# Kernel tuning notes

Hardware: AMD Instinct MI355X
Metric: run time of the kernel (lower is better)

## Reference

```python
import jax, jax.numpy as jnp
import numpy as np

LATENT, ACTION, HIDDEN, TEMB = 256, 32, 1024, 128
BATCH, NTRAJ, HORIZON = 1024, 16, 5
EPI_W, PRAG_W, CONS_W, GAMMA = 1.0, 1.0, 0.1, 0.99
LOG2PI = float(np.log(2.0 * np.pi))


def _dense_init(key, fan_in, fan_out):
    return jax.random.normal(key, (fan_in, fan_out), dtype=jnp.float32) / np.sqrt(fan_in)


def time_embed(t):
    # sinusoidal embedding, TEMB dims, like ValueNetwork(time_embed_dim=128)
    half = TEMB // 2
    freqs = jnp.exp(-np.log(10000.0) * jnp.arange(half, dtype=jnp.float32) / half)
    ang = t[:, None] * freqs[None, :]  # [B, half]
    return jnp.concatenate([jnp.sin(ang), jnp.cos(ang)], axis=-1)  # [B, TEMB]


def setup_inputs() -> dict:
    key = jax.random.key(0)
    ks = jax.random.split(key, 12)
    return {
        "latent": jax.random.normal(ks[0], (BATCH, LATENT), dtype=jnp.float32),
        "noise": jax.random.normal(ks[1], (NTRAJ, HORIZON, BATCH, ACTION), dtype=jnp.float32),
        # DiffusionConditionedPolicy (state-dependent std): trunk + mean/log_std heads
        "pW1": _dense_init(ks[2], LATENT, HIDDEN), "pb1": jnp.zeros((HIDDEN,), jnp.float32),
        "pW2": _dense_init(ks[3], HIDDEN, HIDDEN), "pb2": jnp.zeros((HIDDEN,), jnp.float32),
        "pWm": _dense_init(ks[4], HIDDEN, ACTION), "pbm": jnp.zeros((ACTION,), jnp.float32),
        "pWs": _dense_init(ks[5], HIDDEN, ACTION), "pbs": jnp.zeros((ACTION,), jnp.float32),
        # LatentDynamicsModel: 3-layer MLP on [latent, action] -> delta
        "dW1": _dense_init(ks[6], LATENT + ACTION, HIDDEN), "db1": jnp.zeros((HIDDEN,), jnp.float32),
        "dW2": _dense_init(ks[7], HIDDEN, HIDDEN), "db2": jnp.zeros((HIDDEN,), jnp.float32),
        "dW3": _dense_init(ks[8], HIDDEN, LATENT), "db3": jnp.zeros((LATENT,), jnp.float32),
        # ValueNetwork: 3-layer MLP on [latent, time_embed] -> scalar
        "vW1": _dense_init(ks[9], LATENT + TEMB, HIDDEN), "vb1": jnp.zeros((HIDDEN,), jnp.float32),
        "vW2": _dense_init(ks[10], HIDDEN, HIDDEN), "vb2": jnp.zeros((HIDDEN,), jnp.float32),
        "vW3": _dense_init(ks[11], HIDDEN, 1), "vb3": jnp.zeros((1,), jnp.float32),
    }


def _efe_forward(latent, noise, pW1, pb1, pW2, pb2, pWm, pbm, pWs, pbs,
                 dW1, db1, dW2, db2, dW3, db3, vW1, vb1, vW2, vb2, vW3, vb3):
    def policy(z, eps):
        h = jax.nn.silu(z @ pW1 + pb1)
        h = jax.nn.silu(h @ pW2 + pb2)
        mean = h @ pWm + pbm
        log_std = jnp.clip(h @ pWs + pbs, -5.0, 2.0)
        action = mean + jnp.exp(log_std) * eps  # reparameterized sample
        # Normal entropy per-dim, summed over action dim
        ent = jnp.sum(0.5 * (1.0 + LOG2PI) + log_std, axis=-1)
        return action, ent

    def dynamics(z, a):
        h = jnp.concatenate([z, a], axis=-1)
        h = jax.nn.silu(h @ dW1 + db1)
        h = jax.nn.silu(h @ dW2 + db2)
        return h @ dW3 + db3  # delta latent

    def value(z, tvec):
        h = jnp.concatenate([z, time_embed(tvec)], axis=-1)
        h = jax.nn.silu(h @ vW1 + vb1)
        h = jax.nn.silu(h @ vW2 + vb2)
        return (h @ vW3 + vb3)[..., 0]  # squeeze(-1)

    def step(z, inp):
        eps_t, t = inp
        action, ent = policy(z, eps_t)
        z_next = z + dynamics(z, action)  # predict_next_latent
        # _compute_latent_kl on normalized latents
        zn = z / (jnp.linalg.norm(z, axis=-1, keepdims=True) + 1e-8)
        pn = z_next / (jnp.linalg.norm(z_next, axis=-1, keepdims=True) + 1e-8)
        kl = 0.5 * jnp.sum((zn - pn) ** 2, axis=-1)
        epistemic = jnp.log1p(kl)
        tvec = jnp.full((z.shape[0],), 0.0, dtype=z.dtype) + t
        pragmatic = value(z_next, tvec)
        consistency = -ent
        step_efe = EPI_W * epistemic + PRAG_W * pragmatic + CONS_W * consistency
        return z_next, step_efe

    ts = jnp.arange(HORIZON, dtype=jnp.float32)

    def rollout(eps_traj):  # eps_traj: [H, B, A]
        _, efes = jax.lax.scan(step, latent, (eps_traj, ts))  # efes: [H, B]
        disc = GAMMA ** ts  # discount_factor ** t
        return jnp.sum(disc[:, None] * efes, axis=0)  # traj_efe: [B]

    traj_efe = jax.vmap(rollout)(noise)  # [NTRAJ, B]
    total_efe = jnp.mean(traj_efe, axis=0)  # sum of traj_efe / num_trajectories
    return total_efe


def reference(latent, noise, pW1, pb1, pW2, pb2, pWm, pbm, pWs, pbs,
              dW1, db1, dW2, db2, dW3, db3, vW1, vb1, vW2, vb2, vW3, vb3):
    return _efe_forward(latent, noise, pW1, pb1, pW2, pb2, pWm, pbm, pWs, pbs,
                        dW1, db1, dW2, db2, dW3, db3, vW1, vb1, vW2, vb2, vW3, vb3)
```

## Files before the change

kernel.cpp:

```cpp
#include <hip/hip_runtime.h>
#include <cstdint>
#include <cstddef>
#include <cmath>


typedef __bf16 bf16;
typedef __attribute__((ext_vector_type(8))) __bf16 bf16x8;
typedef __attribute__((ext_vector_type(4))) __bf16 bf16x4;
typedef __attribute__((ext_vector_type(4))) float f32x4;

static constexpr int BATCH = 1024, NTRAJ = 16, HORIZON = 5;
static constexpr int MR = NTRAJ * BATCH;
static constexpr float ENT_C = 1.4189385332046727f;
static constexpr float SUMDISC = 4.90099501f;

__device__ __forceinline__ void gld_lds16(const bf16* g, const bf16* l) {
  typedef __attribute__((address_space(1))) const uint32_t gq_t;
  typedef __attribute__((address_space(3))) uint32_t lq_t;
  gq_t* gp = (gq_t*)(uintptr_t)g;
  lq_t* lp = (lq_t*)(uint32_t)(uintptr_t)l;
  __builtin_amdgcn_global_load_lds(gp, lp, 16, 0, 0);
}

__device__ __forceinline__ float silu(float x) {
  return x * __builtin_amdgcn_rcpf(1.f + __expf(-x));
}

#define MFMA16(a, b, c) __builtin_amdgcn_mfma_f32_16x16x32_bf16((a), (b), (c), 0, 0, 0)

__global__ __launch_bounds__(256) void gemm128(
    const bf16* __restrict__ A, int lda, int K, const bf16* __restrict__ Bt,
    const float* __restrict__ bias, int act_cols,
    bf16* __restrict__ C1, bf16* __restrict__ C2, int ldc) {
  __shared__ alignas(16) bf16 As0[128 * 32], As1[128 * 32];
  __shared__ alignas(16) bf16 Bs0[128 * 32], Bs1[128 * 32];
  const int tid = threadIdx.x, wave = tid >> 6, lane = tid & 63;
  const int quad = lane >> 4, l16 = lane & 15;
  const int rowBlk = blockIdx.x * 128, colBlk = blockIdx.y * 128;
  const int wr = wave >> 1, wc = wave & 1;
  const int srow = lane >> 2;
  const int skel = (((lane & 3) ^ ((lane >> 3) & 3)) * 8);
  const int qsw = quad ^ ((l16 >> 1) & 3);

  const bf16* gA0 = A + (size_t)(rowBlk + wave * 32 + srow) * lda + skel;
  const bf16* gA1 = gA0 + (size_t)16 * lda;
  const bf16* gB0 = Bt + (size_t)(colBlk + wave * 32 + srow) * K + skel;
  const bf16* gB1 = gB0 + (size_t)16 * K;
  bf16* const lA0 = As0 + wave * 32 * 32;
  bf16* const lA0b = As0 + (wave * 32 + 16) * 32;
  bf16* const lA1 = As1 + wave * 32 * 32;
  bf16* const lA1b = As1 + (wave * 32 + 16) * 32;
  bf16* const lB0 = Bs0 + wave * 32 * 32;
  bf16* const lB0b = Bs0 + (wave * 32 + 16) * 32;
  bf16* const lB1 = Bs1 + wave * 32 * 32;
  bf16* const lB1b = Bs1 + (wave * 32 + 16) * 32;

  f32x4 acc[4][4] = {};
  for (int k0 = 0; k0 < K; k0 += 64) {
    gld_lds16(gA0 + k0, lA0);
    gld_lds16(gA1 + k0, lA0b);
    gld_lds16(gA0 + k0 + 32, lA1);
    gld_lds16(gA1 + k0 + 32, lA1b);
    gld_lds16(gB0 + k0, lB0);
    gld_lds16(gB1 + k0, lB0b);
    gld_lds16(gB0 + k0 + 32, lB1);
    gld_lds16(gB1 + k0 + 32, lB1b);
    __syncthreads();
#pragma unroll
    for (int ks = 0; ks < 2; ++ks) {
      const bf16* aRd = (ks ? As1 : As0) + (wr * 64 + l16) * 32 + qsw * 8;
      const bf16* bRd = (ks ? Bs1 : Bs0) + (wc * 64 + l16) * 32 + qsw * 8;
      bf16x8 af[4], bfr[4];
#pragma unroll
      for (int i = 0; i < 4; ++i) {
        af[i] = *(const bf16x8*)(aRd + i * 16 * 32);
        bfr[i] = *(const bf16x8*)(bRd + i * 16 * 32);
      }
#pragma unroll
      for (int mi = 0; mi < 4; ++mi)
#pragma unroll
        for (int ni = 0; ni < 4; ++ni)
          acc[mi][ni] = MFMA16(bfr[ni], af[mi], acc[mi][ni]);
    }
    __syncthreads();
  }

  const bool doAct = (colBlk < act_cols);
  bf16* const Cp = doAct ? C1 : C2;
  const int cShift = doAct ? 0 : act_cols;
#pragma unroll
  for (int mi = 0; mi < 4; ++mi) {
    const int row = rowBlk + wr * 64 + mi * 16 + l16;
#pragma unroll
    for (int ni = 0; ni < 4; ++ni) {
      const int col0 = colBlk + wc * 64 + ni * 16 + quad * 4;
      const f32x4 bb = *(const f32x4*)(bias + col0);
      bf16x4 o;
#pragma unroll
      for (int r = 0; r < 4; ++r) {
        float x = acc[mi][ni][r] + bb[r];
        if (doAct) x = silu(x);
        o[r] = (bf16)x;
      }
      *(bf16x4*)(Cp + (size_t)row * ldc + (col0 - cShift)) = o;
    }
  }
}

__global__ __launch_bounds__(256) void gemm_pd1v(
    const bf16* __restrict__ A, const bf16* __restrict__ Bt,
    const float* __restrict__ pdb1, const float* __restrict__ vbiasT,
    bf16* __restrict__ Ha, bf16* __restrict__ Hp, bf16* __restrict__ Hv) {
  __shared__ alignas(16) bf16 As0[128 * 32], As1[128 * 32];
  __shared__ alignas(16) bf16 Bs0[128 * 32], Bs1[128 * 32];
  const int tid = threadIdx.x, wave = tid >> 6, lane = tid & 63;
  const int quad = lane >> 4, l16 = lane & 15;
  const int rowBlk = blockIdx.x * 128, colBlk = blockIdx.y * 128;
  const int wr = wave >> 1, wc = wave & 1;
  const int srow = lane >> 2;
  const int skel = (((lane & 3) ^ ((lane >> 3) & 3)) * 8);
  const int qsw = quad ^ ((l16 >> 1) & 3);

  const bf16* gA0 = A + (size_t)(rowBlk + wave * 32 + srow) * 256 + skel;
  const bf16* gA1 = gA0 + (size_t)16 * 256;
  const bf16* gB0 = Bt + (size_t)(colBlk + wave * 32 + srow) * 256 + skel;
  const bf16* gB1 = gB0 + (size_t)16 * 256;
  bf16* const lA0 = As0 + wave * 32 * 32;
  bf16* const lA0b = As0 + (wave * 32 + 16) * 32;
  bf16* const lA1 = As1 + wave * 32 * 32;
  bf16* const lA1b = As1 + (wave * 32 + 16) * 32;
  bf16* const lB0 = Bs0 + wave * 32 * 32;
  bf16* const lB0b = Bs0 + (wave * 32 + 16) * 32;
  bf16* const lB1 = Bs1 + wave * 32 * 32;
  bf16* const lB1b = Bs1 + (wave * 32 + 16) * 32;

  f32x4 acc[4][4] = {};
  for (int k0 = 0; k0 < 256; k0 += 64) {
    gld_lds16(gA0 + k0, lA0);
    gld_lds16(gA1 + k0, lA0b);
    gld_lds16(gA0 + k0 + 32, lA1);
    gld_lds16(gA1 + k0 + 32, lA1b);
    gld_lds16(gB0 + k0, lB0);
    gld_lds16(gB1 + k0, lB0b);
    gld_lds16(gB0 + k0 + 32, lB1);
    gld_lds16(gB1 + k0 + 32, lB1b);
    __syncthreads();
#pragma unroll
    for (int ks = 0; ks < 2; ++ks) {
      const bf16* aRd = (ks ? As1 : As0) + (wr * 64 + l16) * 32 + qsw * 8;
      const bf16* bRd = (ks ? Bs1 : Bs0) + (wc * 64 + l16) * 32 + qsw * 8;
      bf16x8 af[4], bfr[4];
#pragma unroll
      for (int i = 0; i < 4; ++i) {
        af[i] = *(const bf16x8*)(aRd + i * 16 * 32);
        bfr[i] = *(const bf16x8*)(bRd + i * 16 * 32);
      }
#pragma unroll
      for (int mi = 0; mi < 4; ++mi)
#pragma unroll
        for (int ni = 0; ni < 4; ++ni)
          acc[mi][ni] = MFMA16(bfr[ni], af[mi], acc[mi][ni]);
    }
    __syncthreads();
  }

  const int seg = colBlk >> 10;
  bf16* const Cp = (seg == 0) ? Ha : (seg == 1) ? Hp : Hv;
  const int cShift = seg << 10;
  const float* const bp = (seg == 2) ? (vbiasT - 2048) : pdb1;
#pragma unroll
  for (int mi = 0; mi < 4; ++mi) {
    const int row = rowBlk + wr * 64 + mi * 16 + l16;
#pragma unroll
    for (int ni = 0; ni < 4; ++ni) {
      const int col0 = colBlk + wc * 64 + ni * 16 + quad * 4;
      const f32x4 bb = *(const f32x4*)(bp + col0);
      bf16x4 o;
#pragma unroll
      for (int r = 0; r < 4; ++r) {
        float x = acc[mi][ni][r] + bb[r];
        if (seg != 1) x = silu(x);
        o[r] = (bf16)x;
      }
      *(bf16x4*)(Cp + (size_t)row * 1024 + (col0 - cShift)) = o;
    }
  }
}

template <int NT, int EPI>
__global__ __launch_bounds__(512, 2) void gemm256(
    const bf16* __restrict__ A, const bf16* __restrict__ Bt, int nCol,
    const float* __restrict__ bias, const float* __restrict__ aux,
    bf16* __restrict__ C1, float* __restrict__ efe, float disc) {
  static_assert(NT >= 2, "need at least 2 K-tiles");
  constexpr int K = NT * 64;
  __shared__ alignas(16) bf16 sAB[2][2][256 * 64];

  const int tid = threadIdx.x, wave = tid >> 6, lane = tid & 63;
  const int quad = lane >> 4, l16 = lane & 15;
  const int wr = wave >> 2, wc = wave & 3;

  const int nwg = gridDim.x, flat = blockIdx.x;
  const int lid = (flat & 7) * (nwg >> 3) + (flat >> 3);
  const int rowBlk = (lid / nCol) * 256, colBlk = (lid % nCol) * 256;

  const int j8 = lane >> 3;
  const int c16e = ((lane & 7) ^ j8) * 8;
  const bf16* gAs = A + (size_t)(rowBlk + wave * 16 + j8) * K + c16e;
  const bf16* gBs = Bt + (size_t)(colBlk + wave * 16 + j8) * K + c16e;

#define STAGE_A(hh, tt, bb)                                           \
  do {                                                                \
    const bf16* g_ = gAs + (hh) * 128 * K + (tt) * 64;                \
    bf16* l_ = &sAB[(bb)][0][((hh) * 128 + wave * 16) * 64];          \
    gld_lds16(g_, l_);                                                \
    gld_lds16(g_ + 8 * K, l_ + 8 * 64);                               \
  } while (0)
#define STAGE_B(hh, tt, bb)                                           \
  do {                                                                \
    const bf16* g_ = gBs + (hh) * 128 * K + (tt) * 64;                \
    bf16* l_ = &sAB[(bb)][1][((hh) * 128 + wave * 16) * 64];          \
    gld_lds16(g_, l_);                                                \
    gld_lds16(g_ + 8 * K, l_ + 8 * 64);                               \
  } while (0)

  const int k0x = (quad * 8) ^ ((l16 & 7) << 3);
  const int aOff = (wr * 128 + l16) * 64 + k0x;
  const int bOff = (wc * 64 + l16) * 64 + k0x;

  bf16x8 bAf[4][2], bBf[2][2], bB2f[2][2];
  f32x4 acc[8][4] = {};

  STAGE_A(0, 0, 0);
  STAGE_A(1, 0, 0);
  STAGE_B(0, 0, 0);
  STAGE_B(1, 0, 0);
  STAGE_B(0, 1, 1);
  STAGE_B(1, 1, 1);
  asm volatile("s_waitcnt vmcnt(4)" ::: "memory");
  __builtin_amdgcn_s_barrier();
  __builtin_amdgcn_sched_barrier(0);

#pragma unroll 2
  for (int t = 0; t < NT; ++t) {
    const int buf = t & 1;
    const bf16* lA = &sAB[buf][0][0];
    const bf16* lB = &sAB[buf][1][0];

#pragma unroll
    for (int m = 0; m < 4; ++m)
#pragma unroll
      for (int ks = 0; ks < 2; ++ks)
        bAf[m][ks] = *(const bf16x8*)(lA + ((aOff + m * 1024) ^ (ks << 5)));
#pragma unroll
    for (int n = 0; n < 2; ++n)
#pragma unroll
      for (int ks = 0; ks < 2; ++ks)
        bBf[n][ks] = *(const bf16x8*)(lB + ((bOff + n * 1024) ^ (ks << 5)));
    if (t + 1 < NT) STAGE_A(0, t + 1, buf ^ 1);
    __builtin_amdgcn_s_barrier();
    asm volatile("s_waitcnt lgkmcnt(0)" ::: "memory");
    __builtin_amdgcn_sched_barrier(0);
    __builtin_amdgcn_s_setprio(1);
#pragma unroll
    for (int ks = 0; ks < 2; ++ks)
#pragma unroll
      for (int m = 0; m < 4; ++m)
#pragma unroll
        for (int n = 0; n < 2; ++n)
          acc[m][n] = MFMA16(bBf[n][ks], bAf[m][ks], acc[m][n]);
    __builtin_amdgcn_s_setprio(0);
    __builtin_amdgcn_s_barrier();
    __builtin_amdgcn_sched_barrier(0);

#pragma unroll
    for (int n = 0; n < 2; ++n)
#pragma unroll
      for (int ks = 0; ks < 2; ++ks)
        bB2f[n][ks] =
            *(const bf16x8*)(lB + ((bOff + (n + 2) * 1024) ^ (ks << 5)));
    if (t + 1 < NT) STAGE_A(1, t + 1, buf ^ 1);
    __builtin_amdgcn_s_barrier();
    asm volatile("s_waitcnt lgkmcnt(0)" ::: "memory");
    __builtin_amdgcn_sched_barrier(0);
    __builtin_amdgcn_s_setprio(1);
#pragma unroll
    for (int ks = 0; ks < 2; ++ks)
#pragma unroll
      for (int m = 0; m < 4; ++m)
#pragma unroll
        for (int n = 0; n < 2; ++n)
          acc[m][n + 2] = MFMA16(bB2f[n][ks], bAf[m][ks], acc[m][n + 2]);
    __builtin_amdgcn_s_setprio(0);
    __builtin_amdgcn_s_barrier();
    __builtin_amdgcn_sched_barrier(0);

#pragma unroll
    for (int m = 0; m < 4; ++m)
#pragma unroll
      for (int ks = 0; ks < 2; ++ks)
        bAf[m][ks] =
            *(const bf16x8*)(lA + ((aOff + (m + 4) * 1024) ^ (ks << 5)));
    if (t + 2 < NT) STAGE_B(0, t + 2, buf);
    __builtin_amdgcn_s_barrier();
    asm volatile("s_waitcnt lgkmcnt(0)" ::: "memory");
    __builtin_amdgcn_sched_barrier(0);
    __builtin_amdgcn_s_setprio(1);
#pragma unroll
    for (int ks = 0; ks < 2; ++ks)
#pragma unroll
      for (int m = 0; m < 4; ++m)
#pragma unroll
        for (int n = 0; n < 2; ++n)
          acc[m + 4][n + 2] =
              MFMA16(bB2f[n][ks], bAf[m][ks], acc[m + 4][n + 2]);
    __builtin_amdgcn_s_setprio(0);
    __builtin_amdgcn_s_barrier();
    __builtin_amdgcn_sched_barrier(0);

    if (t + 2 < NT) STAGE_B(1, t + 2, buf);
    __builtin_amdgcn_s_barrier();
    __builtin_amdgcn_sched_barrier(0);
    __builtin_amdgcn_s_setprio(1);
#pragma unroll
    for (int ks = 0; ks < 2; ++ks)
#pragma unroll
      for (int m = 0; m < 4; ++m)
#pragma unroll
        for (int n = 0; n < 2; ++n)
          acc[m + 4][n] = MFMA16(bBf[n][ks], bAf[m][ks], acc[m + 4][n]);
    __builtin_amdgcn_s_setprio(0);
    if (t < NT - 2)
      asm volatile("s_waitcnt vmcnt(4)" ::: "memory");
    else
      asm volatile("s_waitcnt vmcnt(0)" ::: "memory");
    __builtin_amdgcn_s_barrier();
    __builtin_amdgcn_sched_barrier(0);
  }
#undef STAGE_A
#undef STAGE_B

  if constexpr (EPI == 0) {
#pragma unroll
    for (int m = 0; m < 8; ++m) {
      const int row = rowBlk + wr * 128 + m * 16 + l16;
#pragma unroll
      for (int n = 0; n < 4; ++n) {
        const int gcol = colBlk + wc * 64 + n * 16 + quad * 4;
        const f32x4 bb = *(const f32x4*)(bias + gcol);
        bf16x4 o;
#pragma unroll
        for (int r = 0; r < 4; ++r) o[r] = (bf16)silu(acc[m][n][r] + bb[r]);
        *(bf16x4*)(C1 + (size_t)row * 1024 + gcol) = o;
      }
    }
  } else {
#pragma unroll
    for (int m = 0; m < 8; ++m) {
      const int row = rowBlk + wr * 128 + m * 16 + l16;
      float p = 0.f;
#pragma unroll
      for (int n = 0; n < 4; ++n) {
        const int gcol = colBlk + wc * 64 + n * 16 + quad * 4;
        const f32x4 bb = *(const f32x4*)(bias + gcol);
        const f32x4 w3 = *(const f32x4*)(aux + gcol);
#pragma unroll
        for (int r = 0; r < 4; ++r) p += silu(acc[m][n][r] + bb[r]) * w3[r];
      }
      p += __shfl_xor(p, 16);
      p += __shfl_xor(p, 32);
      if (quad == 0) atomicAdd(efe + row, disc * p);
    }
  }
}

__global__ __launch_bounds__(256) void gemm_dyn3(
    const bf16* __restrict__ A, const bf16* __restrict__ Bt,
    const float* __restrict__ db3, float* __restrict__ Zf,
    bf16* __restrict__ Zb, float* __restrict__ s_n, float* __restrict__ s_c) {
  __shared__ alignas(16) bf16 As0[64 * 32], As1[64 * 32];
  __shared__ alignas(16) bf16 Bs0[128 * 32], Bs1[128 * 32];
  const int tid = threadIdx.x, wave = tid >> 6, lane = tid & 63;
  const int quad = lane >> 4, l16 = lane & 15;
  const int rowBlk = blockIdx.x * 64, colBlk = blockIdx.y * 128;
  const int srow = lane >> 2;
  const int skel = (((lane & 3) ^ ((lane >> 3) & 3)) * 8);
  const int qsw = quad ^ ((l16 >> 1) & 3);

  const bf16* gA = A + (size_t)(rowBlk + wave * 16 + srow) * 1024 + skel;
  const bf16* gB0 = Bt + (size_t)(colBlk + wave * 32 + srow) * 1024 + skel;
  const bf16* gB1 = gB0 + (size_t)16 * 1024;
  bf16* const lA0 = As0 + wave * 16 * 32;
  bf16* const lA1 = As1 + wave * 16 * 32;
  bf16* const lB0 = Bs0 + wave * 32 * 32;
  bf16* const lB0b = Bs0 + (wave * 32 + 16) * 32;
  bf16* const lB1 = Bs1 + wave * 32 * 32;
  bf16* const lB1b = Bs1 + (wave * 32 + 16) * 32;

  f32x4 acc[8] = {};
  for (int k0 = 0; k0 < 1024; k0 += 64) {
    gld_lds16(gA + k0, lA0);
    gld_lds16(gA + k0 + 32, lA1);
    gld_lds16(gB0 + k0, lB0);
    gld_lds16(gB1 + k0, lB0b);
    gld_lds16(gB0 + k0 + 32, lB1);
    gld_lds16(gB1 + k0 + 32, lB1b);
    __syncthreads();
#pragma unroll
    for (int ks = 0; ks < 2; ++ks) {
      const bf16* aRd = (ks ? As1 : As0) + (wave * 16 + l16) * 32 + qsw * 8;
      const bf16* bRd = (ks ? Bs1 : Bs0) + l16 * 32 + qsw * 8;
      const bf16x8 af = *(const bf16x8*)aRd;
#pragma unroll
      for (int ni = 0; ni < 8; ++ni) {
        const bf16x8 bfr = *(const bf16x8*)(bRd + ni * 16 * 32);
        acc[ni] = MFMA16(bfr, af, acc[ni]);
      }
    }
    __syncthreads();
  }

  const int row = rowBlk + wave * 16 + l16;
  float pn = 0.f, pc = 0.f;
#pragma unroll
  for (int ni = 0; ni < 8; ++ni) {
    const int col0 = colBlk + ni * 16 + quad * 4;
    const f32x4 b4 = *(const f32x4*)(db3 + col0);
    float* zp = Zf + (size_t)row * 256 + col0;
    const f32x4 z = *(const f32x4*)zp;
    f32x4 zn;
    bf16x4 o;
#pragma unroll
    for (int r = 0; r < 4; ++r) {
      zn[r] = z[r] + acc[ni][r] + b4[r];
      pn += zn[r] * zn[r];
      pc += z[r] * zn[r];
      o[r] = (bf16)zn[r];
    }
    *(f32x4*)zp = zn;
    *(bf16x4*)(Zb + (size_t)row * 256 + col0) = o;
  }
  pn += __shfl_xor(pn, 16);
  pn += __shfl_xor(pn, 32);
  pc += __shfl_xor(pc, 16);
  pc += __shfl_xor(pc, 32);
  if (quad == 0) {
    atomicAdd(s_n + row, pn);
    atomicAdd(s_c + row, pc);
  }
}

__global__ void kl_batch(const float* __restrict__ sz0,
                         const float* __restrict__ snAll,
                         const float* __restrict__ scAll,
                         float* __restrict__ efe) {
  const int m = blockIdx.x * 256 + threadIdx.x;
  float sz = sz0[m];
  float disc = 1.f, acc = 0.f;
  for (int t = 0; t < HORIZON; ++t) {
    const float sn = snAll[t * MR + m], sc = scAll[t * MR + m];
    const float nz = sqrtf(sz) + 1e-8f, nn = sqrtf(sn) + 1e-8f;
    const float kl =
        0.5f * (sz / (nz * nz) + sn / (nn * nn) - 2.f * sc / (nz * nn));
    acc += disc * log1pf(fmaxf(kl, 0.f));
    sz = sn;
    disc *= 0.99f;
  }
  efe[m] += acc;
}

__global__ __launch_bounds__(256) void heads4(
    const bf16* __restrict__ H, const bf16* __restrict__ Wt,
    const float* __restrict__ pbm, const float* __restrict__ pbs,
    const float* __restrict__ noise, const bf16* __restrict__ preD,
    const bf16* __restrict__ dW1at, bf16* __restrict__ Hd,
    float* __restrict__ efe, int t, float disc, int rmask) {
  __shared__ alignas(16) bf16 As[4 * 16 * 32];
  __shared__ alignas(16) bf16 Bs[4 * 64 * 32];
  __shared__ alignas(16) bf16 LAct[16 * 32];
  const int tid = threadIdx.x, wave = tid >> 6, lane = tid & 63;
  const int quad = lane >> 4, l16 = lane & 15;
  const int rowBlk = blockIdx.x * 16;
  const int srow = lane >> 2;
  const int skel = (((lane & 3) ^ ((lane >> 3) & 3)) * 8);
  const int qsw = quad ^ ((l16 >> 1) & 3);
  const int kw = wave * 256;

  const bf16* gA = H + (size_t)((rowBlk + srow) & rmask) * 1024 + kw + skel;
  bf16* const lA = As + wave * 16 * 32;
  bf16* const lB = Bs + wave * 64 * 32;

  f32x4 acc[4] = {};
  for (int k0 = 0; k0 < 256; k0 += 32) {
    gld_lds16(gA + k0, lA);
#pragma unroll
    for (int j = 0; j < 4; ++j)
      gld_lds16(Wt + (size_t)(j * 16 + srow) * 1024 + kw + k0 + skel,
                lB + j * 16 * 32);
    __syncthreads();
    const bf16x8 af = *(const bf16x8*)(lA + l16 * 32 + qsw * 8);
#pragma unroll
    for (int ni = 0; ni < 4; ++ni) {
      const bf16x8 bfr = *(const bf16x8*)(lB + (ni * 16 + l16) * 32 + qsw * 8);
      acc[ni] = MFMA16(bfr, af, acc[ni]);
    }
    __syncthreads();
  }

  float* red = (float*)Bs;
#pragma unroll
  for (int ni = 0; ni < 4; ++ni)
    *(f32x4*)(red + wave * 1024 + ni * 256 + lane * 4) = acc[ni];
  __syncthreads();
#pragma unroll
  for (int ni = 0; ni < 4; ++ni) {
    f32x4 s = *(const f32x4*)(red + ni * 256 + lane * 4);
#pragma unroll
    for (int w2 = 1; w2 < 4; ++w2) {
      const f32x4 p = *(const f32x4*)(red + w2 * 1024 + ni * 256 + lane * 4);
#pragma unroll
      for (int r = 0; r < 4; ++r) s[r] += p[r];
    }
    acc[ni] = s;
  }

  const int row = rowBlk + l16;
  const int n = row >> 10, b = row & 1023;
  float ent = 0.f;
#pragma unroll
  for (int ni = 0; ni < 2; ++ni) {
    const int col0 = ni * 16 + quad * 4;
    const f32x4 bm4 = *(const f32x4*)(pbm + col0);
    const f32x4 bs4 = *(const f32x4*)(pbs + col0);
    const f32x4 ep4 =
        *(const f32x4*)(noise + (((size_t)(n * 5 + t) * 1024 + b) * 32 + col0));
    bf16x4 o;
#pragma unroll
    for (int r = 0; r < 4; ++r) {
      const float mean = acc[ni][r] + bm4[r];
      float ls = acc[ni + 2][r] + bs4[r];
      ls = fminf(fmaxf(ls, -5.f), 2.f);
      o[r] = (bf16)(mean + __expf(ls) * ep4[r]);
      ent += ENT_C + ls;
    }
    if (wave == 0) *(bf16x4*)(LAct + l16 * 32 + col0) = o;
  }
  ent += __shfl_xor(ent, 16);
  ent += __shfl_xor(ent, 32);
  if (wave == 0 && quad == 0) efe[row] += disc * (-0.1f) * ent;
  __syncthreads();

  const int prow = row & rmask;
  const bf16x8 af2 = *(const bf16x8*)(LAct + l16 * 32 + quad * 8);
#pragma unroll 4
  for (int ci = 0; ci < 16; ++ci) {
    const int ct = wave * 16 + ci;
    const bf16x8 wf =
        *(const bf16x8*)(dW1at + (size_t)(ct * 16 + l16) * 32 + quad * 8);
    f32x4 a = {};
    a = MFMA16(wf, af2, a);
    const int col0 = ct * 16 + quad * 4;
    const bf16x4 pd = *(const bf16x4*)(preD + (size_t)prow * 1024 + col0);
    bf16x4 o;
#pragma unroll
    for (int r = 0; r < 4; ++r) o[r] = (bf16)silu(a[r] + (float)pd[r]);
    *(bf16x4*)(Hd + (size_t)row * 1024 + col0) = o;
  }
}

__global__ __launch_bounds__(256) void prep_tr(
    const float* __restrict__ pW1, const float* __restrict__ dW1,
    const float* __restrict__ vW1, const float* __restrict__ pW2,
    const float* __restrict__ dW2, const float* __restrict__ dW3,
    const float* __restrict__ vW2, const float* __restrict__ pWm,
    const float* __restrict__ pWs, const float* __restrict__ pb1,
    const float* __restrict__ db1, const float* __restrict__ vb1,
    const float* __restrict__ latent, bf16* __restrict__ pdW1vt,
    bf16* __restrict__ pW2t, bf16* __restrict__ pHt,
    bf16* __restrict__ dW1at, bf16* __restrict__ dW2t,
    bf16* __restrict__ dW3t, bf16* __restrict__ vW2t,
    float* __restrict__ pdb1, float* __restrict__ vbias,
    float* __restrict__ Zf, bf16* __restrict__ Zb0, float* __restrict__ efe,
    float* __restrict__ sz0, float* __restrict__ snAll,
    float* __restrict__ scAll) {
  int bid = blockIdx.x;
  if (bid == 1072) {
    for (int i = threadIdx.x; i < 2048; i += 256)
      pdb1[i] = (i < 1024) ? pb1[i] : db1[i - 1024];
    return;
  }
  if (bid >= 1073 && bid < 1093) {
    const int idx = (bid - 1073) * 256 + threadIdx.x;
    const int t = idx >> 10, j = idx & 1023;
    float s = vb1[j];
    const float lt = (float)t;
    for (int i = 0; i < 64; ++i) {
      const float f = expf(-9.210340371976184f * (float)i / 64.f);
      const float ang = lt * f;
      s += sinf(ang) * vW1[(size_t)(256 + i) * 1024 + j];
      s += cosf(ang) * vW1[(size_t)(256 + 64 + i) * 1024 + j];
    }
    vbias[idx] = s;
    return;
  }
  if (bid >= 1093) {
    const int wave = threadIdx.x >> 6, lane = threadIdx.x & 63;
    const int row = (bid - 1093) * 4 + wave;
    const f32x4 z = *(const f32x4*)(latent + (size_t)(row & 1023) * 256 + lane * 4);
    *(f32x4*)(Zf + (size_t)row * 256 + lane * 4) = z;
    if (row < 1024) {
      bf16x4 o = {(bf16)z[0], (bf16)z[1], (bf16)z[2], (bf16)z[3]};
      *(bf16x4*)(Zb0 + (size_t)row * 256 + lane * 4) = o;
    }
    float s = z[0] * z[0] + z[1] * z[1] + z[2] * z[2] + z[3] * z[3];
#pragma unroll
    for (int m = 1; m < 64; m <<= 1) s += __shfl_xor(s, m);
    if (lane == 0) {
      sz0[row] = s;
      efe[row] = 0.f;
    }
    if (lane < HORIZON) {
      snAll[lane * MR + row] = 0.f;
      scAll[lane * MR + row] = 0.f;
    }
    return;
  }
  const float* in;
  bf16* out;
  int K, N, ldin, ro = 0;
  if (bid < 64) { in = pW1; out = pdW1vt; K = 256; N = 1024; ldin = 1024; }
  else if (bid < 128) { bid -= 64; in = dW1; out = pdW1vt + 1024 * 256; K = 256; N = 1024; ldin = 1024; }
  else if (bid < 192) { bid -= 128; in = vW1; out = pdW1vt + 2048 * 256; K = 256; N = 1024; ldin = 1024; }
  else if (bid < 448) { bid -= 192; in = pW2; out = pW2t; K = 1024; N = 1024; ldin = 1024; }
  else if (bid < 704) { bid -= 448; in = dW2; out = dW2t; K = 1024; N = 1024; ldin = 1024; }
  else if (bid < 960) { bid -= 704; in = vW2; out = vW2t; K = 1024; N = 1024; ldin = 1024; }
  else if (bid < 1024) { bid -= 960; in = dW3; out = dW3t; K = 1024; N = 256; ldin = 256; }
  else if (bid < 1040) { bid -= 1024; in = dW1; out = dW1at; K = 32; N = 1024; ldin = 1024; ro = 256; }
  else if (bid < 1056) { bid -= 1040; in = pWm; out = pHt; K = 1024; N = 32; ldin = 32; }
  else { bid -= 1056; in = pWs; out = pHt + 32 * 1024; K = 1024; N = 32; ldin = 32; }

  const int ktiles = (K + 63) >> 6;
  const int k0 = (bid % ktiles) * 64, n0 = (bid / ktiles) * 64;
  __shared__ float tile[64][65];
  const int tx = threadIdx.x & 63, ty = threadIdx.x >> 6;
#pragma unroll
  for (int i = 0; i < 16; ++i) {
    const int k = k0 + ty + i * 4;
    if (k < K && n0 + tx < N)
      tile[ty + i * 4][tx] = in[(size_t)(ro + k) * ldin + n0 + tx];
  }
  __syncthreads();
#pragma unroll
  for (int i = 0; i < 16; ++i) {
    const int n = n0 + ty + i * 4;
    if (n < N && k0 + tx < K)
      out[(size_t)n * K + k0 + tx] = (bf16)tile[tx][ty + i * 4];
  }
}

__global__ void finalize(const float* __restrict__ efe,
                         const float* __restrict__ vb3,
                         float* __restrict__ out) {
  const int b = blockIdx.x * 256 + threadIdx.x;
  float s = 0.f;
#pragma unroll
  for (int n = 0; n < 16; ++n) s += efe[n * 1024 + b];
  out[b] = s * (1.f / 16.f) + SUMDISC * vb3[0];
}

extern "C" void kernel_launch(void* const* d_in, const int* in_sizes, int n_in,
                              void* d_out, int out_size, void* d_ws,
                              size_t ws_size, hipStream_t stream) {
  const float* latent = (const float*)d_in[0];
  const float* noise = (const float*)d_in[1];
  const float* pW1 = (const float*)d_in[2];
  const float* pb1 = (const float*)d_in[3];
  const float* pW2 = (const float*)d_in[4];
  const float* pb2 = (const float*)d_in[5];
  const float* pWm = (const float*)d_in[6];
  const float* pbm = (const float*)d_in[7];
  const float* pWs = (const float*)d_in[8];
  const float* pbs = (const float*)d_in[9];
  const float* dW1 = (const float*)d_in[10];
  const float* db1 = (const float*)d_in[11];
  const float* dW2 = (const float*)d_in[12];
  const float* db2 = (const float*)d_in[13];
  const float* dW3 = (const float*)d_in[14];
  const float* db3 = (const float*)d_in[15];
  const float* vW1 = (const float*)d_in[16];
  const float* vb1 = (const float*)d_in[17];
  const float* vW2 = (const float*)d_in[18];
  const float* vb2 = (const float*)d_in[19];
  const float* vW3 = (const float*)d_in[20];
  const float* vb3 = (const float*)d_in[21];

  char* w = (char*)d_ws;
  size_t off = 0;
  auto take = [&](size_t bytes) -> void* {
    void* p = (void*)(w + off);
    off = (off + bytes + 255) & ~(size_t)255;
    return p;
  };
  bf16* pdW1vt = (bf16*)take(3072ull * 256 * 2);
  float* pdb1 = (float*)take(2048ull * 4);
  bf16* pW2t = (bf16*)take(1024ull * 1024 * 2);
  bf16* pHt = (bf16*)take(64ull * 1024 * 2);
  bf16* dW1at = (bf16*)take(1024ull * 32 * 2);
  bf16* dW2t = (bf16*)take(1024ull * 1024 * 2);
  bf16* dW3t = (bf16*)take(256ull * 1024 * 2);
  bf16* vW2t = (bf16*)take(1024ull * 1024 * 2);
  float* vbias = (float*)take(5ull * 1024 * 4);
  bf16* Zb0 = (bf16*)take(1024ull * 256 * 2);
  bf16* Zb = (bf16*)take((size_t)MR * 256 * 2);
  float* Zf = (float*)take((size_t)MR * 256 * 4);
  float* efe = (float*)take((size_t)MR * 4);
  float* sz0 = (float*)take((size_t)MR * 4);
  float* snAll = (float*)take(5ull * MR * 4);
  float* scAll = (float*)take(5ull * MR * 4);
  bf16* Ha = (bf16*)take((size_t)MR * 1024 * 2);
  bf16* Hc = (bf16*)take((size_t)MR * 1024 * 2);
  bf16* Hp = (bf16*)take((size_t)MR * 1024 * 2);
  bf16* Hv = (bf16*)take((size_t)MR * 1024 * 2);
  bf16* vW1t = pdW1vt + (size_t)2048 * 256;

  const dim3 blk(256), blk2(512);
  const int BIG = 1 << 30;
  prep_tr<<<dim3(1093 + MR / 4), blk, 0, stream>>>(
      pW1, dW1, vW1, pW2, dW2, dW3, vW2, pWm, pWs, pb1, db1, vb1, latent,
      pdW1vt, pW2t, pHt, dW1at, dW2t, dW3t, vW2t, pdb1, vbias, Zf, Zb0, efe,
      sz0, snAll, scAll);

  float disc = 1.f, dprev = 1.f;
  for (int s = 0; s < HORIZON; ++s) {
    const int rmask = (s == 0) ? 1023 : 0x7FFFFFFF;
    if (s == 0) {
      gemm128<<<dim3(8, 16), blk, 0, stream>>>(Zb0, 256, 256, pdW1vt, pdb1,
                                               1024, Ha, Hp, 1024);
      gemm128<<<dim3(8, 8), blk, 0, stream>>>(Ha, 1024, 1024, pW2t, pb2, BIG,
                                              Hc, Hc, 1024);
    } else {
      gemm_pd1v<<<dim3(128, 24), blk, 0, stream>>>(
          Zb, pdW1vt, pdb1, vbias + (s - 1) * 1024, Ha, Hp, Hv);
      gemm256<16, 0><<<dim3(256), blk2, 0, stream>>>(Ha, pW2t, 4, pb2, nullptr,
                                                     Hc, nullptr, 0.f);
      gemm256<16, 1><<<dim3(256), blk2, 0, stream>>>(Hv, vW2t, 4, vb2, vW3,
                                                     nullptr, efe, dprev);
    }
    heads4<<<dim3(MR / 16), blk, 0, stream>>>(Hc, pHt, pbm, pbs, noise, Hp,
                                              dW1at, Ha, efe, s, disc, rmask);
    gemm256<16, 0><<<dim3(256), blk2, 0, stream>>>(Ha, dW2t, 4, db2, nullptr,
                                                   Hc, nullptr, 0.f);
    gemm_dyn3<<<dim3(MR / 64, 2), blk, 0, stream>>>(
        Hc, dW3t, db3, Zf, Zb, snAll + (size_t)s * MR, scAll + (size_t)s * MR);
    dprev = disc;
    disc *= 0.99f;
  }

  kl_batch<<<dim3(MR / 256), blk, 0, stream>>>(sz0, snAll, scAll, efe);

  gemm128<<<dim3(128, 8), blk, 0, stream>>>(Zb, 256, 256, vW1t,
                                            vbias + 4 * 1024, BIG, Hv, Hv,
                                            1024);
  gemm256<16, 1><<<dim3(256), blk2, 0, stream>>>(Hv, vW2t, 4, vb2, vW3,
                                                 nullptr, efe, dprev);
  finalize<<<dim3(4), blk, 0, stream>>>(efe, vb3, (float*)d_out);
}
```

Measured before the change: 1.072 ms.

## Double-buffer LDS tiles with async global-to-LDS prefetch in three GEMM kernels

Converts the single-stage load-then-compute loops in gemm128, gemm_pd1v and gemm_dyn3 to a two-stage LDS ping-pong. The next k-tile is issued via global_load_lds while the current one is consumed, with explicit vmcnt waits, s_barrier and sched_barrier. The aim is to hide global memory latency behind MFMA work instead of stalling on every tile. LDS usage doubles per block, which may reduce occupancy, and the hand-written waitcnt/barrier ordering is fragile.

```diff
diff --git a/kernel.cpp b/kernel.cpp
--- a/kernel.cpp
+++ b/kernel.cpp
@@ -27,13 +27,16 @@
 }
 
 #define MFMA16(a, b, c) __builtin_amdgcn_mfma_f32_16x16x32_bf16((a), (b), (c), 0, 0, 0)
+#define SBAR() __builtin_amdgcn_s_barrier()
+#define SCHED0() __builtin_amdgcn_sched_barrier(0)
+#define VMCNT(n) asm volatile("s_waitcnt vmcnt(" #n ")" ::: "memory")
 
 __global__ __launch_bounds__(256) void gemm128(
     const bf16* __restrict__ A, int lda, int K, const bf16* __restrict__ Bt,
     const float* __restrict__ bias, int act_cols,
     bf16* __restrict__ C1, bf16* __restrict__ C2, int ldc) {
-  __shared__ alignas(16) bf16 As0[128 * 32], As1[128 * 32];
-  __shared__ alignas(16) bf16 Bs0[128 * 32], Bs1[128 * 32];
+  __shared__ alignas(16) bf16 PA[2][2][128 * 32];
+  __shared__ alignas(16) bf16 PB[2][2][128 * 32];
   const int tid = threadIdx.x, wave = tid >> 6, lane = tid & 63;
   const int quad = lane >> 4, l16 = lane & 15;
   const int rowBlk = blockIdx.x * 128, colBlk = blockIdx.y * 128;
@@ -46,30 +49,33 @@
   const bf16* gA1 = gA0 + (size_t)16 * lda;
   const bf16* gB0 = Bt + (size_t)(colBlk + wave * 32 + srow) * K + skel;
   const bf16* gB1 = gB0 + (size_t)16 * K;
-  bf16* const lA0 = As0 + wave * 32 * 32;
-  bf16* const lA0b = As0 + (wave * 32 + 16) * 32;
-  bf16* const lA1 = As1 + wave * 32 * 32;
-  bf16* const lA1b = As1 + (wave * 32 + 16) * 32;
-  bf16* const lB0 = Bs0 + wave * 32 * 32;
-  bf16* const lB0b = Bs0 + (wave * 32 + 16) * 32;
-  bf16* const lB1 = Bs1 + wave * 32 * 32;
-  bf16* const lB1b = Bs1 + (wave * 32 + 16) * 32;
+
+#define STG128(t, b)                                      \
+  do {                                                    \
+    const int k0_ = (t)*64;                               \
+    gld_lds16(gA0 + k0_, &PA[b][0][wave * 1024]);         \
+    gld_lds16(gA1 + k0_, &PA[b][0][wave * 1024 + 512]);   \
+    gld_lds16(gA0 + k0_ + 32, &PA[b][1][wave * 1024]);    \
+    gld_lds16(gA1 + k0_ + 32, &PA[b][1][wave * 1024 + 512]); \
+    gld_lds16(gB0 + k0_, &PB[b][0][wave * 1024]);         \
+    gld_lds16(gB1 + k0_, &PB[b][0][wave * 1024 + 512]);   \
+    gld_lds16(gB0 + k0_ + 32, &PB[b][1][wave * 1024]);    \
+    gld_lds16(gB1 + k0_ + 32, &PB[b][1][wave * 1024 + 512]); \
+  } while (0)
 
   f32x4 acc[4][4] = {};
-  for (int k0 = 0; k0 < K; k0 += 64) {
-    gld_lds16(gA0 + k0, lA0);
-    gld_lds16(gA1 + k0, lA0b);
-    gld_lds16(gA0 + k0 + 32, lA1);
-    gld_lds16(gA1 + k0 + 32, lA1b);
-    gld_lds16(gB0 + k0, lB0);
-    gld_lds16(gB1 + k0, lB0b);
-    gld_lds16(gB0 + k0 + 32, lB1);
-    gld_lds16(gB1 + k0 + 32, lB1b);
-    __syncthreads();
+  const int nt = K >> 6;
+  STG128(0, 0);
+  STG128(1, 1);
+  VMCNT(8);
+  SBAR();
+  SCHED0();
+  for (int t = 0; t < nt; ++t) {
+    const int b = t & 1;
 #pragma unroll
     for (int ks = 0; ks < 2; ++ks) {
-      const bf16* aRd = (ks ? As1 : As0) + (wr * 64 + l16) * 32 + qsw * 8;
-      const bf16* bRd = (ks ? Bs1 : Bs0) + (wc * 64 + l16) * 32 + qsw * 8;
+      const bf16* aRd = &PA[b][ks][(wr * 64 + l16) * 32 + qsw * 8];
+      const bf16* bRd = &PB[b][ks][(wc * 64 + l16) * 32 + qsw * 8];
       bf16x8 af[4], bfr[4];
 #pragma unroll
       for (int i = 0; i < 4; ++i) {
@@ -82,8 +88,19 @@
         for (int ni = 0; ni < 4; ++ni)
           acc[mi][ni] = MFMA16(bfr[ni], af[mi], acc[mi][ni]);
     }
-    __syncthreads();
-  }
+    if (t == nt - 1) break;
+    SBAR();
+    SCHED0();
+    if (t + 2 < nt) {
+      STG128(t + 2, b);
+      VMCNT(8);
+    } else {
+      VMCNT(0);
+    }
+    SBAR();
+    SCHED0();
+  }
+#undef STG128
 
   const bool doAct = (colBlk < act_cols);
   bf16* const Cp = doAct ? C1 : C2;
@@ -111,8 +128,8 @@
     const bf16* __restrict__ A, const bf16* __restrict__ Bt,
     const float* __restrict__ pdb1, const float* __restrict__ vbiasT,
     bf16* __restrict__ Ha, bf16* __restrict__ Hp, bf16* __restrict__ Hv) {
-  __shared__ alignas(16) bf16 As0[128 * 32], As1[128 * 32];
-  __shared__ alignas(16) bf16 Bs0[128 * 32], Bs1[128 * 32];
+  __shared__ alignas(16) bf16 PA[2][2][128 * 32];
+  __shared__ alignas(16) bf16 PB[2][2][128 * 32];
   const int tid = threadIdx.x, wave = tid >> 6, lane = tid & 63;
   const int quad = lane >> 4, l16 = lane & 15;
   const int rowBlk = blockIdx.x * 128, colBlk = blockIdx.y * 128;
@@ -125,30 +142,33 @@
   const bf16* gA1 = gA0 + (size_t)16 * 256;
   const bf16* gB0 = Bt + (size_t)(colBlk + wave * 32 + srow) * 256 + skel;
   const bf16* gB1 = gB0 + (size_t)16 * 256;
-  bf16* const lA0 = As0 + wave * 32 * 32;
-  bf16* const lA0b = As0 + (wave * 32 + 16) * 32;
-  bf16* const lA1 = As1 + wave * 32 * 32;
-  bf16* const lA1b = As1 + (wave * 32 + 16) * 32;
-  bf16* const lB0 = Bs0 + wave * 32 * 32;
-  bf16* const lB0b = Bs0 + (wave * 32 + 16) * 32;
-  bf16* const lB1 = Bs1 + wave * 32 * 32;
-  bf16* const lB1b = Bs1 + (wave * 32 + 16) * 32;
+
+#define STGP(t, b)                                        \
+  do {                                                    \
+    const int k0_ = (t)*64;                               \
+    gld_lds16(gA0 + k0_, &PA[b][0][wave * 1024]);         \
+    gld_lds16(gA1 + k0_, &PA[b][0][wave * 1024 + 512]);   \
+    gld_lds16(gA0 + k0_ + 32, &PA[b][1][wave * 1024]);    \
+    gld_lds16(gA1 + k0_ + 32, &PA[b][1][wave * 1024 + 512]); \
+    gld_lds16(gB0 + k0_, &PB[b][0][wave * 1024]);         \
+    gld_lds16(gB1 + k0_, &PB[b][0][wave * 1024 + 512]);   \
+    gld_lds16(gB0 + k0_ + 32, &PB[b][1][wave * 1024]);    \
+    gld_lds16(gB1 + k0_ + 32, &PB[b][1][wave * 1024 + 512]); \
+  } while (0)
 
   f32x4 acc[4][4] = {};
-  for (int k0 = 0; k0 < 256; k0 += 64) {
-    gld_lds16(gA0 + k0, lA0);
-    gld_lds16(gA1 + k0, lA0b);
-    gld_lds16(gA0 + k0 + 32, lA1);
-    gld_lds16(gA1 + k0 + 32, lA1b);
-    gld_lds16(gB0 + k0, lB0);
-    gld_lds16(gB1 + k0, lB0b);
-    gld_lds16(gB0 + k0 + 32, lB1);
-    gld_lds16(gB1 + k0 + 32, lB1b);
-    __syncthreads();
+  STGP(0, 0);
+  STGP(1, 1);
+  VMCNT(8);
+  SBAR();
+  SCHED0();
+#pragma unroll
+  for (int t = 0; t < 4; ++t) {
+    const int b = t & 1;
 #pragma unroll
     for (int ks = 0; ks < 2; ++ks) {
-      const bf16* aRd = (ks ? As1 : As0) + (wr * 64 + l16) * 32 + qsw * 8;
-      const bf16* bRd = (ks ? Bs1 : Bs0) + (wc * 64 + l16) * 32 + qsw * 8;
+      const bf16* aRd = &PA[b][ks][(wr * 64 + l16) * 32 + qsw * 8];
+      const bf16* bRd = &PB[b][ks][(wc * 64 + l16) * 32 + qsw * 8];
       bf16x8 af[4], bfr[4];
 #pragma unroll
       for (int i = 0; i < 4; ++i) {
@@ -161,8 +181,19 @@
         for (int ni = 0; ni < 4; ++ni)
           acc[mi][ni] = MFMA16(bfr[ni], af[mi], acc[mi][ni]);
     }
-    __syncthreads();
-  }
+    if (t == 3) break;
+    SBAR();
+    SCHED0();
+    if (t < 2) {
+      STGP(t + 2, b);
+      VMCNT(8);
+    } else {
+      VMCNT(0);
+    }
+    SBAR();
+    SCHED0();
+  }
+#undef STGP
 
   const int seg = colBlk >> 10;
   bf16* const Cp = (seg == 0) ? Ha : (seg == 1) ? Hp : Hv;
@@ -378,8 +409,8 @@
     const bf16* __restrict__ A, const bf16* __restrict__ Bt,
     const float* __restrict__ db3, float* __restrict__ Zf,
     bf16* __restrict__ Zb, float* __restrict__ s_n, float* __restrict__ s_c) {
-  __shared__ alignas(16) bf16 As0[64 * 32], As1[64 * 32];
-  __shared__ alignas(16) bf16 Bs0[128 * 32], Bs1[128 * 32];
+  __shared__ alignas(16) bf16 PA[2][2][64 * 32];
+  __shared__ alignas(16) bf16 PB[2][2][128 * 32];
   const int tid = threadIdx.x, wave = tid >> 6, lane = tid & 63;
   const int quad = lane >> 4, l16 = lane & 15;
   const int rowBlk = blockIdx.x * 64, colBlk = blockIdx.y * 128;
@@ -390,26 +421,31 @@
   const bf16* gA = A + (size_t)(rowBlk + wave * 16 + srow) * 1024 + skel;
   const bf16* gB0 = Bt + (size_t)(colBlk + wave * 32 + srow) * 1024 + skel;
   const bf16* gB1 = gB0 + (size_t)16 * 1024;
-  bf16* const lA0 = As0 + wave * 16 * 32;
-  bf16* const lA1 = As1 + wave * 16 * 32;
-  bf16* const lB0 = Bs0 + wave * 32 * 32;
-  bf16* const lB0b = Bs0 + (wave * 32 + 16) * 32;
-  bf16* const lB1 = Bs1 + wave * 32 * 32;
-  bf16* const lB1b = Bs1 + (wave * 32 + 16) * 32;
+
+#define STGD(t, b)                                        \
+  do {                                                    \
+    const int k0_ = (t)*64;                               \
+    gld_lds16(gA + k0_, &PA[b][0][wave * 512]);           \
+    gld_lds16(gA + k0_ + 32, &PA[b][1][wave * 512]);      \
+    gld_lds16(gB0 + k0_, &PB[b][0][wave * 1024]);         \
+    gld_lds16(gB1 + k0_, &PB[b][0][wave * 1024 + 512]);   \
+    gld_lds16(gB0 + k0_ + 32, &PB[b][1][wave * 1024]);    \
+    gld_lds16(gB1 + k0_ + 32, &PB[b][1][wave * 1024 + 512]); \
+  } while (0)
 
   f32x4 acc[8] = {};
-  for (int k0 = 0; k0 < 1024; k0 += 64) {
-    gld_lds16(gA + k0, lA0);
-    gld_lds16(gA + k0 + 32, lA1);
-    gld_lds16(gB0 + k0, lB0);
-    gld_lds16(gB1 + k0, lB0b);
-    gld_lds16(gB0 + k0 + 32, lB1);
-    gld_lds16(gB1 + k0 + 32, lB1b);
-    __syncthreads();
+  STGD(0, 0);
+  STGD(1, 1);
+  VMCNT(6);
+  SBAR();
+  SCHED0();
+#pragma unroll 2
+  for (int t = 0; t < 16; ++t) {
+    const int b = t & 1;
 #pragma unroll
     for (int ks = 0; ks < 2; ++ks) {
-      const bf16* aRd = (ks ? As1 : As0) + (wave * 16 + l16) * 32 + qsw * 8;
-      const bf16* bRd = (ks ? Bs1 : Bs0) + l16 * 32 + qsw * 8;
+      const bf16* aRd = &PA[b][ks][(wave * 16 + l16) * 32 + qsw * 8];
+      const bf16* bRd = &PB[b][ks][l16 * 32 + qsw * 8];
       const bf16x8 af = *(const bf16x8*)aRd;
 #pragma unroll
       for (int ni = 0; ni < 8; ++ni) {
@@ -417,8 +453,19 @@
         acc[ni] = MFMA16(bfr, af, acc[ni]);
       }
     }
-    __syncthreads();
-  }
+    if (t == 15) break;
+    SBAR();
+    SCHED0();
+    if (t < 14) {
+      STGD(t + 2, b);
+      VMCNT(6);
+    } else {
+      VMCNT(0);
+    }
+    SBAR();
+    SCHED0();
+  }
+#undef STGD
 
   const int row = rowBlk + wave * 16 + l16;
   float pn = 0.f, pc = 0.f;
```

Result: no change. 1.061 ms (-1.0%).
